# Kernel optimization log

Hardware: AMD Instinct MI355X
Metric: run time of the kernel (lower is better)

The kernel has to match this reference:

```python
import math
import jax, jax.numpy as jnp
from jax import lax
import numpy as np

LN_EPS = 1e-5
K = 3          # deform-conv kernel size
PAD = 1        # 'same' padding so offset map matches output resolution


def setup_inputs() -> dict:
    key = jax.random.key(0)
    ks = jax.random.split(key, 6)
    B, C, H, W, Co = 4, 256, 64, 64, 256
    x = jax.random.normal(ks[0], (B, C, H, W), jnp.float32)
    dwc_w = jax.random.normal(ks[1], (C, 1, K, K), jnp.float32) * 0.02
    ln_w = jnp.ones((C,), jnp.float32)
    ln_b = jnp.zeros((C,), jnp.float32)
    fcd_w = jax.random.normal(ks[2], (1, C, 1, 1), jnp.float32) * 0.02
    fca_w = jax.random.normal(ks[3], (1, C, 1, 1), jnp.float32) * 0.02
    fan_in = C * K * K
    dconv_w = jax.random.normal(ks[4], (Co, C, K, K), jnp.float32) / math.sqrt(fan_in)
    dconv_b = jnp.zeros((Co,), jnp.float32)
    return dict(x=x, dwc_w=dwc_w, ln_w=ln_w, ln_b=ln_b,
                fcd_w=fcd_w, fca_w=fca_w, dconv_w=dconv_w, dconv_b=dconv_b)


def _bilinear_sample(x, py, px):
    # x: [B,C,H,W]; py/px: [B,KK,H,W] float sample positions (zero-padded border)
    B, C, H, W = x.shape
    y0 = jnp.floor(py); x0 = jnp.floor(px)
    y1 = y0 + 1.0;      x1 = x0 + 1.0
    wy1 = py - y0; wy0 = 1.0 - wy1
    wx1 = px - x0; wx0 = 1.0 - wx1

    def gather(yy, xx):
        valid = ((yy >= 0) & (yy < H) & (xx >= 0) & (xx < W)).astype(x.dtype)
        iy = jnp.clip(yy, 0, H - 1).astype(jnp.int32)
        ix = jnp.clip(xx, 0, W - 1).astype(jnp.int32)
        # per-batch fancy gather -> [B,C,KK,H,W]
        v = jax.vmap(lambda img, a, b: img[:, a, b])(x, iy, ix)
        return v * valid[:, None]

    return (gather(y0, x0) * (wy0 * wx0)[:, None]
          + gather(y0, x1) * (wy0 * wx1)[:, None]
          + gather(y1, x0) * (wy1 * wx0)[:, None]
          + gather(y1, x1) * (wy1 * wx1)[:, None])


def reference(x, dwc_w, ln_w, ln_b, fcd_w, fca_w, dconv_w, dconv_b):
    B, C, H, W = x.shape
    KK = K * K
    # --- offset branch ---
    h = lax.conv_general_dilated(x, dwc_w, (1, 1), ((1, 1), (1, 1)),
                                 dimension_numbers=('NCHW', 'OIHW', 'NCHW'),
                                 feature_group_count=C)
    mu = h.mean(axis=1, keepdims=True)
    var = h.var(axis=1, keepdims=True)
    h = (h - mu) * lax.rsqrt(var + LN_EPS)
    h = h * ln_w[None, :, None, None] + ln_b[None, :, None, None]
    h = jax.nn.relu(h)
    r = jax.nn.relu(jnp.einsum('bchw,oc->bohw', h, fcd_w[:, :, 0, 0]))      # [B,1,H,W]
    t = jnp.einsum('bchw,oc->bohw', h, fca_w[:, :, 0, 0])
    theta = (t / (1.0 + jnp.abs(t))) * (math.pi / 180.0)                     # softsign * pi/180
    ox = r * jnp.cos(theta)
    oy = r * jnp.sin(theta)
    # torch code: offsets = cat([ox tiled KK, oy tiled KK], dim=1) -> [B,2KK,H,W]
    off = jnp.concatenate([jnp.tile(ox, (1, KK, 1, 1)), jnp.tile(oy, (1, KK, 1, 1))], axis=1)
    # torchvision DeformConv2d convention: channel 2k = dy, channel 2k+1 = dx
    dy = off[:, 0::2]   # [B,KK,H,W]
    dx = off[:, 1::2]
    # --- deformable sampling ---
    ky = jnp.repeat(jnp.arange(K), K).astype(x.dtype)   # kernel row per tap
    kx = jnp.tile(jnp.arange(K), K).astype(x.dtype)     # kernel col per tap
    py = (jnp.arange(H, dtype=x.dtype) - PAD)[None, None, :, None] + ky[None, :, None, None] + dy
    px = (jnp.arange(W, dtype=x.dtype) - PAD)[None, None, None, :] + kx[None, :, None, None] + dx
    sampled = _bilinear_sample(x, py, px)               # [B,C,KK,H,W]
    Co = dconv_w.shape[0]
    out = jnp.einsum('bckhw,ock->bohw', sampled, dconv_w.reshape(Co, C, KK))
    return out + dconv_b[None, :, None, None]
```

## Files before the change

kernel.cpp:

```cpp
#include <hip/hip_runtime.h>
#include <hip/hip_bf16.h>

#define B_   4
#define C_   256
#define CO_  256
#define H_   64
#define W_   64
#define HW_  4096

typedef __attribute__((ext_vector_type(8))) short short8;
typedef __attribute__((ext_vector_type(4))) float f32x4;
typedef __attribute__((ext_vector_type(2))) float f32x2;

static __device__ __forceinline__ unsigned short f2bf(float f) {
    unsigned u = __builtin_bit_cast(unsigned, f);
    unsigned r = (u + 0x7fffu + ((u >> 16) & 1u)) >> 16;
    return (unsigned short)r;
}
static __device__ __forceinline__ f32x2 pk_mul(f32x2 a, f32x2 b) {
    f32x2 d; asm("v_pk_mul_f32 %0, %1, %2" : "=v"(d) : "v"(a), "v"(b)); return d;
}
static __device__ __forceinline__ f32x2 pk_fma(f32x2 a, f32x2 b, f32x2 c) {
    f32x2 d; asm("v_pk_fma_f32 %0, %1, %2, %3" : "=v"(d) : "v"(a), "v"(b), "v"(c)); return d;
}
static __device__ __forceinline__ f32x2 pk_add(f32x2 a, f32x2 b) {
    f32x2 d; asm("v_pk_add_f32 %0, %1, %2" : "=v"(d) : "v"(a), "v"(b)); return d;
}
static __device__ __forceinline__ unsigned cvtpk(float a, float b) {
    unsigned r; asm("v_cvt_pk_bf16_f32 %0, %1, %2" : "=v"(r) : "v"(a), "v"(b)); return r;
}
static __device__ __forceinline__ f32x2 unpack_bf2(unsigned d) {
    f32x2 v;
    v.x = __builtin_bit_cast(float, d << 16);
    v.y = __builtin_bit_cast(float, d & 0xffff0000u);
    return v;
}

__global__ void k_pre(const float* __restrict__ x, unsigned short* __restrict__ xT,
                      const float* __restrict__ w, unsigned short* __restrict__ Bt,
                      const float* __restrict__ dwc_w, float* __restrict__ dwcT)
{
    int bid = blockIdx.x;
    int tid = threadIdx.x;
    if (bid < 1024) {
        __shared__ float t[32][132];
        int b   = bid >> 8;
        int rem = bid & 255;
        int hwT = rem >> 1, cT = rem & 1;
        int hw0 = hwT * 32, c0 = cT * 128;
        const float* src = x + (size_t)b * C_ * HW_;
        {
            int hw4 = (tid & 7) << 2;
            int cr  = tid >> 3;
#pragma unroll
            for (int it = 0; it < 4; ++it) {
                int c = cr + it * 32;
                f32x4 v = *(const f32x4*)(src + (size_t)(c0 + c) * HW_ + hw0 + hw4);
                t[hw4 + 0][c] = v.x;
                t[hw4 + 1][c] = v.y;
                t[hw4 + 2][c] = v.z;
                t[hw4 + 3][c] = v.w;
            }
        }
        __syncthreads();
        {
            int c8  = (tid & 15) << 3;
            int hwr = tid >> 4;
            unsigned short* dst = xT + (size_t)(((b << 12) + hw0) * 256) + c0 + c8;
#pragma unroll
            for (int it = 0; it < 2; ++it) {
                int hw = hwr + it * 16;
                f32x4 va = *(const f32x4*)&t[hw][c8];
                f32x4 vb = *(const f32x4*)&t[hw][c8 + 4];
                uint4 u;
                u.x = cvtpk(va.x, va.y);
                u.y = cvtpk(va.z, va.w);
                u.z = cvtpk(vb.x, vb.y);
                u.w = cvtpk(vb.z, vb.w);
                *(uint4*)(dst + (size_t)hw * 256) = u;
            }
        }
    } else {
        int pb = bid - 1024;
        if (pb < 9) dwcT[pb * 256 + tid] = dwc_w[tid * 9 + pb];
        int e = pb * 256 + tid;
        int j   = e & 7;
        int l4  = (e >> 3) & 3;
        int l15 = (e >> 5) & 15;
        int ks  = (e >> 9) & 7;
        int og  = (e >> 12) & 15;
        int k   = e >> 16;
        int o = og * 16 + l15;
        int c = ks * 32 + l4 * 8 + j;
        Bt[e] = f2bf(w[(o * C_ + c) * 9 + k]);
    }
}

__global__ void k_offsets(const unsigned short* __restrict__ xT,
                          const float* __restrict__ dwcT,
                          const float* __restrict__ ln_w,
                          const float* __restrict__ ln_b,
                          const float* __restrict__ fcd_w,
                          const float* __restrict__ fca_w,
                          float* __restrict__ OX, float* __restrict__ OY)
{
    int tid = threadIdx.x;
    int bi = blockIdx.x;
    int g = ((bi & 7) << 6) | (bi >> 3);
    int p0 = g << 5;
    int b = p0 >> 12;
    int y = (p0 >> 6) & 63;
    int xh = p0 & 63;
    int gpos = tid >> 4;
    int csub = tid & 15;
    int ch0 = csub << 4;
    const unsigned short* xb = xT + (size_t)b * HW_ * C_;

    f32x2 acc2[8];
#pragma unroll
    for (int i = 0; i < 8; ++i) { acc2[i].x = 0.f; acc2[i].y = 0.f; }
#pragma unroll
    for (int j = 0; j < 9; ++j) {
        int gy = y + j / 3 - 1, gx = xh + gpos + j % 3 - 1;
        if (gy >= 0 && gy < H_ && gx >= 0 && gx < W_) {
            const unsigned short* p = xb + (size_t)((gy << 6) + gx) * 256 + ch0;
            short8 rlo = *(const short8*)(p);
            short8 rhi = *(const short8*)(p + 8);
            const float* wrow = dwcT + j * 256 + ch0;
#pragma unroll
            for (int q = 0; q < 4; ++q) {
                f32x4 wv = *(const f32x4*)(wrow + q * 4);
                f32x2 w01v; w01v.x = wv.x; w01v.y = wv.y;
                f32x2 w23v; w23v.x = wv.z; w23v.y = wv.w;
                unsigned lo = (q < 2) ? ((unsigned*)&rlo)[q * 2] : ((unsigned*)&rhi)[(q - 2) * 2];
                unsigned hi = (q < 2) ? ((unsigned*)&rlo)[q * 2 + 1] : ((unsigned*)&rhi)[(q - 2) * 2 + 1];
                acc2[q * 2 + 0] = pk_fma(unpack_bf2(lo), w01v, acc2[q * 2 + 0]);
                acc2[q * 2 + 1] = pk_fma(unpack_bf2(hi), w23v, acc2[q * 2 + 1]);
            }
        }
    }
    f32x2 sum2, sq2;
    sum2.x = 0.f; sum2.y = 0.f; sq2.x = 0.f; sq2.y = 0.f;
#pragma unroll
    for (int i = 0; i < 8; ++i) {
        sum2 = pk_add(sum2, acc2[i]);
        sq2  = pk_fma(acc2[i], acc2[i], sq2);
    }
    float s1 = sum2.x + sum2.y, s2 = sq2.x + sq2.y;
#pragma unroll
    for (int m = 1; m <= 8; m <<= 1) {
        s1 += __shfl_xor(s1, m);
        s2 += __shfl_xor(s2, m);
    }
    float mu  = s1 * (1.f / 256.f);
    float var = s2 * (1.f / 256.f) - mu * mu;
    float rs  = rsqrtf(var + 1e-5f);
    float d1 = 0.f, d2 = 0.f;
#pragma unroll
    for (int q = 0; q < 4; ++q) {
        f32x4 lwv = *(const f32x4*)(ln_w  + ch0 + q * 4);
        f32x4 lbv = *(const f32x4*)(ln_b  + ch0 + q * 4);
        f32x4 fdv = *(const f32x4*)(fcd_w + ch0 + q * 4);
        f32x4 fav = *(const f32x4*)(fca_w + ch0 + q * 4);
#pragma unroll
        for (int i = 0; i < 4; ++i) {
            float av = (i & 1) ? acc2[q * 2 + (i >> 1)].y : acc2[q * 2 + (i >> 1)].x;
            float hn = (av - mu) * rs * lwv[i] + lbv[i];
            hn = fmaxf(hn, 0.f);
            d1 = fmaf(hn, fdv[i], d1);
            d2 = fmaf(hn, fav[i], d2);
        }
    }
#pragma unroll
    for (int m = 1; m <= 8; m <<= 1) {
        d1 += __shfl_xor(d1, m);
        d2 += __shfl_xor(d2, m);
    }
    if (csub == 0) {
        float r0 = fmaxf(d1, 0.f);
        float theta = d2 / (1.f + fabsf(d2)) * 0.017453292519943295f;
        int pos = p0 + gpos;
        OX[pos] = r0 * cosf(theta);
        OY[pos] = r0 * sinf(theta);
    }
}

__launch_bounds__(512, 2)
__global__ void k_main(const unsigned short* __restrict__ xT,
                       const float* __restrict__ OX, const float* __restrict__ OY,
                       const unsigned short* __restrict__ Bt,
                       const float* __restrict__ bias,
                       float* __restrict__ out)
{
    __shared__ __align__(16) unsigned char smem[65536];

    int tid = threadIdx.x;
    int bi = blockIdx.x;
    int tile = ((bi & 7) << 5) | (bi >> 3);
    int b = tile >> 6;
    int y = tile & 63;

    int lane = tid & 63, wid = tid >> 6;
    int l15 = lane & 15, l4 = lane >> 4;

    f32x4 acc[4][2];
#pragma unroll
    for (int m = 0; m < 4; ++m)
#pragma unroll
        for (int n = 0; n < 2; ++n) {
            acc[m][n].x = 0.f; acc[m][n].y = 0.f; acc[m][n].z = 0.f; acc[m][n].w = 0.f;
        }

    int gpos = tid >> 3;
    unsigned csub = (unsigned)tid & 7u;
    const char* xbB = (const char*)(xT + (size_t)b * HW_ * C_);
    const unsigned short* bwave = Bt + (unsigned)(wid * 2) * 4096u
                                     + (unsigned)(l15 * 32 + l4 * 8);
    unsigned rowb = (unsigned)gpos * 256u;
    unsigned wsl0 = (csub ^ ((unsigned)gpos & 15u)) << 4;
    unsigned wsl1 = ((8u + csub) ^ ((unsigned)gpos & 15u)) << 4;
    float ox = OX[(tile << 6) + gpos], oy = OY[(tile << 6) + gpos];

    unsigned o00, o01, o10, o11;
    f32x2 W00, W01, W10, W11;

#define GADDR(k)                                                                  \
    {   int ky = (k) / 3, kx = (k) - ky * 3;                                      \
        float dyv = ((k) <= 4) ? ox : oy;                                         \
        float dxv = ((k) <= 3) ? ox : oy;                                         \
        float py = (float)(y - 1 + ky) + dyv;                                     \
        float px = (float)(gpos - 1 + kx) + dxv;                                  \
        float y0f = floorf(py), x0f = floorf(px);                                 \
        int y0 = (int)y0f, x0 = (int)x0f;                                         \
        int y1 = y0 + 1, x1 = x0 + 1;                                             \
        float wy1 = py - y0f, wy0 = 1.f - wy1;                                    \
        float wx1 = px - x0f, wx0 = 1.f - wx1;                                    \
        float vy0 = (y0 >= 0 && y0 < H_) ? 1.f : 0.f;                             \
        float vy1 = (y1 >= 0 && y1 < H_) ? 1.f : 0.f;                             \
        float vx0 = (x0 >= 0 && x0 < W_) ? 1.f : 0.f;                             \
        float vx1 = (x1 >= 0 && x1 < W_) ? 1.f : 0.f;                             \
        float w00 = wy0 * wx0 * vy0 * vx0, w01 = wy0 * wx1 * vy0 * vx1;           \
        float w10 = wy1 * wx0 * vy1 * vx0, w11 = wy1 * wx1 * vy1 * vx1;           \
        W00.x = w00; W00.y = w00; W01.x = w01; W01.y = w01;                       \
        W10.x = w10; W10.y = w10; W11.x = w11; W11.y = w11;                       \
        int y0c = min(max(y0, 0), H_ - 1), y1c = min(max(y1, 0), H_ - 1);         \
        int x0c = min(max(x0, 0), W_ - 1), x1c = min(max(x1, 0), W_ - 1);         \
        unsigned cb = csub << 4;                                                  \
        o00 = (unsigned)((y0c << 6) + x0c) * 512u + cb;                           \
        o01 = (unsigned)((y0c << 6) + x1c) * 512u + cb;                           \
        o10 = (unsigned)((y1c << 6) + x0c) * 512u + cb;                           \
        o11 = (unsigned)((y1c << 6) + x1c) * 512u + cb;                           \
    }

#define GATHER_HALF(h, hbase)                                                     \
    {   _Pragma("unroll")                                                         \
        for (int cq2 = 0; cq2 < 2; ++cq2) {                                       \
            unsigned gb = (unsigned)(h) * 256u + (unsigned)cq2 * 128u;            \
            short8 r00 = *(const short8*)(xbB + o00 + gb);                        \
            short8 r01 = *(const short8*)(xbB + o01 + gb);                        \
            short8 r10 = *(const short8*)(xbB + o10 + gb);                        \
            short8 r11 = *(const short8*)(xbB + o11 + gb);                        \
            uint4 pkv;                                                            \
            _Pragma("unroll")                                                     \
            for (int dw = 0; dw < 4; ++dw) {                                      \
                f32x2 a2 = pk_mul(unpack_bf2(((unsigned*)&r00)[dw]), W00);        \
                a2 = pk_fma(unpack_bf2(((unsigned*)&r01)[dw]), W01, a2);          \
                a2 = pk_fma(unpack_bf2(((unsigned*)&r10)[dw]), W10, a2);          \
                a2 = pk_fma(unpack_bf2(((unsigned*)&r11)[dw]), W11, a2);          \
                ((unsigned*)&pkv)[dw] = cvtpk(a2.x, a2.y);                        \
            }                                                                     \
            *(uint4*)(smem + (hbase) + rowb + (cq2 ? wsl1 : wsl0)) = pkv;         \
        }                                                                         \
    }

#define MFMA_HALF(k, h, hbase)                                                    \
    {   const unsigned short* bk = bwave + (unsigned)(k) * 65536u;                \
        _Pragma("unroll")                                                         \
        for (int ks2 = 0; ks2 < 4; ++ks2) {                                       \
            int ks = (h) * 4 + ks2;                                               \
            short8 bf0 = *(const short8*)(bk + ks * 512);                         \
            short8 bf1 = *(const short8*)(bk + 4096 + ks * 512);                  \
            unsigned sl = ((unsigned)(ks2 * 4 + l4) ^ (unsigned)l15) << 4;        \
            _Pragma("unroll")                                                     \
            for (int mf = 0; mf < 4; ++mf) {                                      \
                unsigned row = (unsigned)(mf * 16 + l15);                         \
                short8 a = *(const short8*)(smem + (hbase) + row * 256u + sl);    \
                acc[mf][0] = __builtin_amdgcn_mfma_f32_16x16x32_bf16(a, bf0, acc[mf][0], 0, 0, 0); \
                acc[mf][1] = __builtin_amdgcn_mfma_f32_16x16x32_bf16(a, bf1, acc[mf][1], 0, 0, 0); \
            }                                                                     \
        }                                                                         \
    }

    GADDR(0);
    GATHER_HALF(0, 0u);
    GATHER_HALF(1, 16384u);
    __syncthreads();

#pragma unroll
    for (int k = 0; k < 9; ++k) {
        unsigned cur = (k & 1) ? 32768u : 0u;
        unsigned nxt = (k & 1) ? 0u : 32768u;
        if (k < 8) {
            GADDR(k + 1);
            GATHER_HALF(0, nxt);
            GATHER_HALF(1, nxt + 16384u);
        }
        MFMA_HALF(k, 0, cur);
        MFMA_HALF(k, 1, cur + 16384u);
        __syncthreads();
    }

#pragma unroll
    for (int nf = 0; nf < 2; ++nf) {
        int col = wid * 32 + nf * 16 + l15;
        float bv = bias[col];
        float* obase = out + ((size_t)(b * CO_ + col)) * HW_ + (y << 6);
#pragma unroll
        for (int mf = 0; mf < 4; ++mf) {
            f32x4 v;
            v.x = acc[mf][nf].x + bv;
            v.y = acc[mf][nf].y + bv;
            v.z = acc[mf][nf].z + bv;
            v.w = acc[mf][nf].w + bv;
            *(f32x4*)(obase + mf * 16 + l4 * 4) = v;
        }
    }
}

extern "C" void kernel_launch(void* const* d_in, const int* in_sizes, int n_in,
                              void* d_out, int out_size, void* d_ws, size_t ws_size,
                              hipStream_t stream) {
    const float* x      = (const float*)d_in[0];
    const float* dwc_w  = (const float*)d_in[1];
    const float* ln_w   = (const float*)d_in[2];
    const float* ln_b   = (const float*)d_in[3];
    const float* fcd_w  = (const float*)d_in[4];
    const float* fca_w  = (const float*)d_in[5];
    const float* dconv_w= (const float*)d_in[6];
    const float* dconv_b= (const float*)d_in[7];
    float* out = (float*)d_out;

    unsigned char* ws = (unsigned char*)d_ws;
    unsigned short* xT = (unsigned short*)(ws);
    unsigned short* Bt = (unsigned short*)(ws + 8388608);
    float* dwcT        = (float*)(ws + 9568256);
    float* OX          = (float*)(ws + 9577472);
    float* OY          = (float*)(ws + 9643008);

    k_pre<<<3328, 256, 0, stream>>>(x, xT, dconv_w, Bt, dwc_w, dwcT);
    k_offsets<<<512, 512, 0, stream>>>(xT, dwcT, ln_w, ln_b, fcd_w, fca_w, OX, OY);
    k_main<<<256, 512, 0, stream>>>(xT, OX, OY, Bt, dconv_b, out);
}
```

Measured before the change: 69.19 us.

## Fuse offset-branch computation into main deformable-conv kernel

Removes the separate k_offsets kernel and computes the depthwise conv, LayerNorm, ReLU, projections and ox/oy per pixel at the start of k_main. Each output-row block now computes its own 64 offsets, with 8 threads per pixel each covering 32 channels. This drops a kernel launch and the OX/OY round trip through global memory. In exchange, k_main runs a serial prologue with more live registers (a 16-entry accumulator) under its 512-thread, 2-block launch bound, and the offset work is spread over fewer blocks.

New measurement: 74.55 us. 7.7% more time.

```diff
diff --git a/kernel.cpp b/kernel.cpp
--- a/kernel.cpp
+++ b/kernel.cpp
@@ -96,98 +96,13 @@
     }
 }
 
-__global__ void k_offsets(const unsigned short* __restrict__ xT,
-                          const float* __restrict__ dwcT,
-                          const float* __restrict__ ln_w,
-                          const float* __restrict__ ln_b,
-                          const float* __restrict__ fcd_w,
-                          const float* __restrict__ fca_w,
-                          float* __restrict__ OX, float* __restrict__ OY)
-{
-    int tid = threadIdx.x;
-    int bi = blockIdx.x;
-    int g = ((bi & 7) << 6) | (bi >> 3);
-    int p0 = g << 5;
-    int b = p0 >> 12;
-    int y = (p0 >> 6) & 63;
-    int xh = p0 & 63;
-    int gpos = tid >> 4;
-    int csub = tid & 15;
-    int ch0 = csub << 4;
-    const unsigned short* xb = xT + (size_t)b * HW_ * C_;
-
-    f32x2 acc2[8];
-#pragma unroll
-    for (int i = 0; i < 8; ++i) { acc2[i].x = 0.f; acc2[i].y = 0.f; }
-#pragma unroll
-    for (int j = 0; j < 9; ++j) {
-        int gy = y + j / 3 - 1, gx = xh + gpos + j % 3 - 1;
-        if (gy >= 0 && gy < H_ && gx >= 0 && gx < W_) {
-            const unsigned short* p = xb + (size_t)((gy << 6) + gx) * 256 + ch0;
-            short8 rlo = *(const short8*)(p);
-            short8 rhi = *(const short8*)(p + 8);
-            const float* wrow = dwcT + j * 256 + ch0;
-#pragma unroll
-            for (int q = 0; q < 4; ++q) {
-                f32x4 wv = *(const f32x4*)(wrow + q * 4);
-                f32x2 w01v; w01v.x = wv.x; w01v.y = wv.y;
-                f32x2 w23v; w23v.x = wv.z; w23v.y = wv.w;
-                unsigned lo = (q < 2) ? ((unsigned*)&rlo)[q * 2] : ((unsigned*)&rhi)[(q - 2) * 2];
-                unsigned hi = (q < 2) ? ((unsigned*)&rlo)[q * 2 + 1] : ((unsigned*)&rhi)[(q - 2) * 2 + 1];
-                acc2[q * 2 + 0] = pk_fma(unpack_bf2(lo), w01v, acc2[q * 2 + 0]);
-                acc2[q * 2 + 1] = pk_fma(unpack_bf2(hi), w23v, acc2[q * 2 + 1]);
-            }
-        }
-    }
-    f32x2 sum2, sq2;
-    sum2.x = 0.f; sum2.y = 0.f; sq2.x = 0.f; sq2.y = 0.f;
-#pragma unroll
-    for (int i = 0; i < 8; ++i) {
-        sum2 = pk_add(sum2, acc2[i]);
-        sq2  = pk_fma(acc2[i], acc2[i], sq2);
-    }
-    float s1 = sum2.x + sum2.y, s2 = sq2.x + sq2.y;
-#pragma unroll
-    for (int m = 1; m <= 8; m <<= 1) {
-        s1 += __shfl_xor(s1, m);
-        s2 += __shfl_xor(s2, m);
-    }
-    float mu  = s1 * (1.f / 256.f);
-    float var = s2 * (1.f / 256.f) - mu * mu;
-    float rs  = rsqrtf(var + 1e-5f);
-    float d1 = 0.f, d2 = 0.f;
-#pragma unroll
-    for (int q = 0; q < 4; ++q) {
-        f32x4 lwv = *(const f32x4*)(ln_w  + ch0 + q * 4);
-        f32x4 lbv = *(const f32x4*)(ln_b  + ch0 + q * 4);
-        f32x4 fdv = *(const f32x4*)(fcd_w + ch0 + q * 4);
-        f32x4 fav = *(const f32x4*)(fca_w + ch0 + q * 4);
-#pragma unroll
-        for (int i = 0; i < 4; ++i) {
-            float av = (i & 1) ? acc2[q * 2 + (i >> 1)].y : acc2[q * 2 + (i >> 1)].x;
-            float hn = (av - mu) * rs * lwv[i] + lbv[i];
-            hn = fmaxf(hn, 0.f);
-            d1 = fmaf(hn, fdv[i], d1);
-            d2 = fmaf(hn, fav[i], d2);
-        }
-    }
-#pragma unroll
-    for (int m = 1; m <= 8; m <<= 1) {
-        d1 += __shfl_xor(d1, m);
-        d2 += __shfl_xor(d2, m);
-    }
-    if (csub == 0) {
-        float r0 = fmaxf(d1, 0.f);
-        float theta = d2 / (1.f + fabsf(d2)) * 0.017453292519943295f;
-        int pos = p0 + gpos;
-        OX[pos] = r0 * cosf(theta);
-        OY[pos] = r0 * sinf(theta);
-    }
-}
-
 __launch_bounds__(512, 2)
 __global__ void k_main(const unsigned short* __restrict__ xT,
-                       const float* __restrict__ OX, const float* __restrict__ OY,
+                       const float* __restrict__ dwcT,
+                       const float* __restrict__ ln_w,
+                       const float* __restrict__ ln_b,
+                       const float* __restrict__ fcd_w,
+                       const float* __restrict__ fca_w,
                        const unsigned short* __restrict__ Bt,
                        const float* __restrict__ bias,
                        float* __restrict__ out)
@@ -203,6 +118,82 @@
     int lane = tid & 63, wid = tid >> 6;
     int l15 = lane & 15, l4 = lane >> 4;
 
+    int gpos = tid >> 3;
+    unsigned csub = (unsigned)tid & 7u;
+    const unsigned short* xb = xT + (size_t)b * HW_ * C_;
+    const char* xbB = (const char*)xb;
+
+    float ox, oy;
+    {
+        int ch0 = (int)csub << 5;
+        f32x2 acc2[16];
+#pragma unroll
+        for (int i = 0; i < 16; ++i) { acc2[i].x = 0.f; acc2[i].y = 0.f; }
+#pragma unroll
+        for (int j = 0; j < 9; ++j) {
+            int gy = y + j / 3 - 1, gx = gpos + j % 3 - 1;
+            if (gy >= 0 && gy < H_ && gx >= 0 && gx < W_) {
+                const unsigned short* p = xb + (size_t)((gy << 6) + gx) * 256 + ch0;
+                const float* wrow = dwcT + j * 256 + ch0;
+#pragma unroll
+                for (int cc = 0; cc < 4; ++cc) {
+                    short8 r = *(const short8*)(p + cc * 8);
+                    f32x4 wa = *(const f32x4*)(wrow + cc * 8);
+                    f32x4 wb2 = *(const f32x4*)(wrow + cc * 8 + 4);
+                    f32x2 wp0; wp0.x = wa.x; wp0.y = wa.y;
+                    f32x2 wp1; wp1.x = wa.z; wp1.y = wa.w;
+                    f32x2 wp2; wp2.x = wb2.x; wp2.y = wb2.y;
+                    f32x2 wp3; wp3.x = wb2.z; wp3.y = wb2.w;
+                    acc2[cc*4+0] = pk_fma(unpack_bf2(((unsigned*)&r)[0]), wp0, acc2[cc*4+0]);
+                    acc2[cc*4+1] = pk_fma(unpack_bf2(((unsigned*)&r)[1]), wp1, acc2[cc*4+1]);
+                    acc2[cc*4+2] = pk_fma(unpack_bf2(((unsigned*)&r)[2]), wp2, acc2[cc*4+2]);
+                    acc2[cc*4+3] = pk_fma(unpack_bf2(((unsigned*)&r)[3]), wp3, acc2[cc*4+3]);
+                }
+            }
+        }
+        f32x2 sum2, sq2;
+        sum2.x = 0.f; sum2.y = 0.f; sq2.x = 0.f; sq2.y = 0.f;
+#pragma unroll
+        for (int i = 0; i < 16; ++i) {
+            sum2 = pk_add(sum2, acc2[i]);
+            sq2  = pk_fma(acc2[i], acc2[i], sq2);
+        }
+        float s1 = sum2.x + sum2.y, s2 = sq2.x + sq2.y;
+#pragma unroll
+        for (int m = 1; m <= 4; m <<= 1) {
+            s1 += __shfl_xor(s1, m);
+            s2 += __shfl_xor(s2, m);
+        }
+        float mu  = s1 * (1.f / 256.f);
+        float var = s2 * (1.f / 256.f) - mu * mu;
+        float rs  = rsqrtf(var + 1e-5f);
+        float d1 = 0.f, d2 = 0.f;
+#pragma unroll
+        for (int q = 0; q < 8; ++q) {
+            f32x4 lwv = *(const f32x4*)(ln_w  + ch0 + q * 4);
+            f32x4 lbv = *(const f32x4*)(ln_b  + ch0 + q * 4);
+            f32x4 fdv = *(const f32x4*)(fcd_w + ch0 + q * 4);
+            f32x4 fav = *(const f32x4*)(fca_w + ch0 + q * 4);
+#pragma unroll
+            for (int i = 0; i < 4; ++i) {
+                float av = (i & 1) ? acc2[q * 2 + (i >> 1)].y : acc2[q * 2 + (i >> 1)].x;
+                float hn = (av - mu) * rs * lwv[i] + lbv[i];
+                hn = fmaxf(hn, 0.f);
+                d1 = fmaf(hn, fdv[i], d1);
+                d2 = fmaf(hn, fav[i], d2);
+            }
+        }
+#pragma unroll
+        for (int m = 1; m <= 4; m <<= 1) {
+            d1 += __shfl_xor(d1, m);
+            d2 += __shfl_xor(d2, m);
+        }
+        float r0 = fmaxf(d1, 0.f);
+        float theta = d2 / (1.f + fabsf(d2)) * 0.017453292519943295f;
+        ox = r0 * cosf(theta);
+        oy = r0 * sinf(theta);
+    }
+
     f32x4 acc[4][2];
 #pragma unroll
     for (int m = 0; m < 4; ++m)
@@ -211,15 +202,11 @@
             acc[m][n].x = 0.f; acc[m][n].y = 0.f; acc[m][n].z = 0.f; acc[m][n].w = 0.f;
         }
 
-    int gpos = tid >> 3;
-    unsigned csub = (unsigned)tid & 7u;
-    const char* xbB = (const char*)(xT + (size_t)b * HW_ * C_);
     const unsigned short* bwave = Bt + (unsigned)(wid * 2) * 4096u
                                      + (unsigned)(l15 * 32 + l4 * 8);
     unsigned rowb = (unsigned)gpos * 256u;
     unsigned wsl0 = (csub ^ ((unsigned)gpos & 15u)) << 4;
     unsigned wsl1 = ((8u + csub) ^ ((unsigned)gpos & 15u)) << 4;
-    float ox = OX[(tile << 6) + gpos], oy = OY[(tile << 6) + gpos];
 
     unsigned o00, o01, o10, o11;
     f32x2 W00, W01, W10, W11;
@@ -344,10 +331,7 @@
     unsigned short* xT = (unsigned short*)(ws);
     unsigned short* Bt = (unsigned short*)(ws + 8388608);
     float* dwcT        = (float*)(ws + 9568256);
-    float* OX          = (float*)(ws + 9577472);
-    float* OY          = (float*)(ws + 9643008);
 
     k_pre<<<3328, 256, 0, stream>>>(x, xT, dconv_w, Bt, dwc_w, dwcT);
-    k_offsets<<<512, 512, 0, stream>>>(xT, dwcT, ln_w, ln_b, fcd_w, fca_w, OX, OY);
-    k_main<<<256, 512, 0, stream>>>(xT, OX, OY, Bt, dconv_b, out);
-}
+    k_main<<<256, 512, 0, stream>>>(xT, dwcT, ln_w, ln_b, fcd_w, fca_w, Bt, dconv_b, out);
+}
```
